# Optimization experiments

Hardware: AMD Instinct MI355X
Metric: run time of the kernel (lower is better)

The kernel has to match this reference:

```python
import jax, jax.numpy as jnp
import numpy as np

EPS = 1e-5

def layer_norm(x, g, b):
    mu = jnp.mean(x, axis=-1, keepdims=True)
    var = jnp.mean(jnp.square(x - mu), axis=-1, keepdims=True)
    return (x - mu) * jax.lax.rsqrt(var + EPS) * g + b

def setup_inputs() -> dict:
    key = jax.random.key(0)
    ks = jax.random.split(key, 8)
    B, N, C, H = 1, 384, 128, 128
    s = 0.02
    return {
        "pair": jax.random.normal(ks[0], (B, N, N, C), dtype=jnp.float32),
        "ln_l_g": jnp.ones((C,), jnp.float32), "ln_l_b": jnp.zeros((C,), jnp.float32),
        "ln_r_g": jnp.ones((C,), jnp.float32), "ln_r_b": jnp.zeros((C,), jnp.float32),
        "Wl": jax.random.normal(ks[1], (C, H), jnp.float32) * s, "bl": jnp.zeros((H,), jnp.float32),
        "Wr": jax.random.normal(ks[2], (C, H), jnp.float32) * s, "br": jnp.zeros((H,), jnp.float32),
        "Wg": jax.random.normal(ks[3], (C, H), jnp.float32) * s, "bg": jnp.zeros((H,), jnp.float32),
        "Wo": jax.random.normal(ks[4], (H, C), jnp.float32) * s, "bo": jnp.zeros((C,), jnp.float32),
        "n_g": jnp.ones((C,), jnp.float32), "n_b": jnp.zeros((C,), jnp.float32),
    }

def reference(pair, ln_l_g, ln_l_b, ln_r_g, ln_r_b, Wl, bl, Wr, br, Wg, bg, Wo, bo, n_g, n_b):
    # pair: [B, N, N, C]
    left = layer_norm(pair, ln_l_g, ln_l_b) @ Wl + bl      # [B,N,N,H]
    right = layer_norm(pair, ln_r_g, ln_r_b) @ Wr + br     # [B,N,N,H]
    gate = jax.nn.sigmoid(pair @ Wg + bg)                  # [B,N,N,H]
    # triangle multiplicative update: per-channel N x N matmul over k
    out = jnp.einsum('bikh,bkjh->bijh', left, right)
    out = out * gate
    out = out @ Wo + bo                                    # [B,N,N,C]
    return layer_norm(out + pair, n_g, n_b)
```

## Files before the change

kernel.cpp:

```cpp
#include <hip/hip_runtime.h>
#include <hip/hip_bf16.h>

#define N_ 384
#define C_ 128
#define M_ (N_*N_)

typedef __attribute__((ext_vector_type(8))) short bf16x8_t;
typedef __attribute__((ext_vector_type(4))) float f32x4_t;
typedef unsigned int u32;
typedef unsigned short u16;
typedef unsigned long long u64;

__device__ __forceinline__ u16 f2bf(float f) {
  u32 u = __builtin_bit_cast(u32, f);
  u32 r = (u + 0x7FFFu + ((u >> 16) & 1u)) >> 16;
  return (u16)r;
}
__device__ __forceinline__ float bf2f(u16 h) {
  u32 u = ((u32)h) << 16;
  return __builtin_bit_cast(float, u);
}

__global__ __launch_bounds__(256) void k_prep1(const float* __restrict__ lg, const float* __restrict__ rg,
    const float* __restrict__ Wl, const float* __restrict__ Wr, const float* __restrict__ Wg,
    const float* __restrict__ Wo, u16* __restrict__ wcat, u16* __restrict__ wot) {
  int idx = blockIdx.x*256 + threadIdx.x;
  if (idx < 49152) {
    int n = idx >> 7, k = idx & 127;
    float v;
    if (n < 128)      v = lg[k] * Wl[k*128 + n];
    else if (n < 256) v = rg[k] * Wr[k*128 + (n-128)];
    else              v = Wg[k*128 + (n-256)];
    wcat[idx] = f2bf(v);
  } else {
    int i2 = idx - 49152;
    int c = i2 >> 7, h = i2 & 127;
    wot[i2] = f2bf(Wo[h*128 + c]);
  }
}

__global__ __launch_bounds__(512) void k_prep2(const float* __restrict__ lb, const float* __restrict__ rb,
    const float* __restrict__ Wl, const float* __restrict__ Wr, const float* __restrict__ Wg,
    const float* __restrict__ bl, const float* __restrict__ br, const float* __restrict__ bg,
    float* __restrict__ bcat, float* __restrict__ sg) {
  int t = threadIdx.x;
  if (blockIdx.x == 0) {
    if (t < 384) {
      float s = 0.f;
      if (t < 128)      { for (int k=0;k<128;k++) s += lb[k]*Wl[k*128+t];       s += bl[t];     }
      else if (t < 256) { int h=t-128; for (int k=0;k<128;k++) s += rb[k]*Wr[k*128+h]; s += br[h]; }
      else              { s = bg[t-256]; }
      bcat[t] = s;
    }
  } else {
    if (t < 128) {
      float s = 0.f;
      for (int k=0;k<128;k++) s += Wg[k*128+t];
      sg[t] = s;
    }
  }
}

#define LDK 136
#define LDA 72
#define LDW 72

__global__ __launch_bounds__(512) void k_projln(const float* __restrict__ pair,
    const u16* __restrict__ wcat, const float* __restrict__ bcat, const float* __restrict__ sg,
    u16* __restrict__ left_t, u16* __restrict__ right_t, u16* __restrict__ gate_t) {
  __shared__ u16 At[128*LDK];
  __shared__ float mu_s[128];
  __shared__ float irs_s[128];
  int bx = blockIdx.x;
  int r0 = bx * 128;
  int t = threadIdx.x, w = t>>6, lane = t&63;
  int q = lane>>4, nl = lane&15;

  {
    int rr = t >> 2, quarter = t & 3;
    const float4* gp = (const float4*)(pair + (size_t)(r0+rr)*128 + quarter*32);
    float4 v[8];
    #pragma unroll
    for (int i=0;i<8;i++) v[i] = gp[i];
    float s=0.f, qq=0.f;
    #pragma unroll
    for (int i=0;i<8;i++) {
      s  += v[i].x + v[i].y + v[i].z + v[i].w;
      qq += v[i].x*v[i].x + v[i].y*v[i].y + v[i].z*v[i].z + v[i].w*v[i].w;
    }
    s  += __shfl_xor(s, 1, 64);
    s  += __shfl_xor(s, 2, 64);
    qq += __shfl_xor(qq, 1, 64);
    qq += __shfl_xor(qq, 2, 64);
    float mu = s * (1.f/128.f);
    float var = qq*(1.f/128.f) - mu*mu;
    float rstd = rsqrtf(var + 1e-5f);
    if (quarter == 0) { mu_s[rr] = mu; irs_s[rr] = 1.0f/rstd; }
    u32* lp = (u32*)(At + rr*LDK + quarter*32);
    #pragma unroll
    for (int i=0;i<4;i++) {
      u32 p0 = (u32)f2bf((v[2*i].x-mu)*rstd)   | ((u32)f2bf((v[2*i].y-mu)*rstd)<<16);
      u32 p1 = (u32)f2bf((v[2*i].z-mu)*rstd)   | ((u32)f2bf((v[2*i].w-mu)*rstd)<<16);
      u32 p2 = (u32)f2bf((v[2*i+1].x-mu)*rstd) | ((u32)f2bf((v[2*i+1].y-mu)*rstd)<<16);
      u32 p3 = (u32)f2bf((v[2*i+1].z-mu)*rstd) | ((u32)f2bf((v[2*i+1].w-mu)*rstd)<<16);
      ((uint4*)lp)[i] = make_uint4(p0,p1,p2,p3);
    }
  }
  __syncthreads();

  #pragma unroll 1
  for (int nb = 0; nb < 3; ++nb) {
    const u16* bbase = wcat + (size_t)(nb*128)*128;
    f32x4_t acc[8] = {};
    #pragma unroll
    for (int ks=0; ks<4; ks++) {
      int kel = ks*32 + q*8;
      bf16x8_t b = *(const bf16x8_t*)(bbase + (size_t)(w*16 + nl)*128 + kel);
      #pragma unroll
      for (int tm=0;tm<8;tm++) {
        bf16x8_t a = *(const bf16x8_t*)(At + (tm*16+nl)*LDK + kel);
        acc[tm] = __builtin_amdgcn_mfma_f32_16x16x32_bf16(a, b, acc[tm], 0,0,0);
      }
    }
    u16* dst = (nb==0) ? left_t : (nb==1) ? right_t : gate_t;
    int n = w*16 + nl;
    float bias = bcat[nb*128 + n];
    u16* rowp = dst + (size_t)n*M_ + r0;
    if (nb == 2) {
      float sgn = sg[n];
      #pragma unroll
      for (int tm=0;tm<8;tm++) {
        f32x4_t mu4 = *(const f32x4_t*)(mu_s  + tm*16 + q*4);
        f32x4_t ir4 = *(const f32x4_t*)(irs_s + tm*16 + q*4);
        float v0 = acc[tm][0]*ir4[0] + mu4[0]*sgn + bias;
        float v1 = acc[tm][1]*ir4[1] + mu4[1]*sgn + bias;
        float v2 = acc[tm][2]*ir4[2] + mu4[2]*sgn + bias;
        float v3 = acc[tm][3]*ir4[3] + mu4[3]*sgn + bias;
        v0 = 1.0f/(1.0f+__expf(-v0));
        v1 = 1.0f/(1.0f+__expf(-v1));
        v2 = 1.0f/(1.0f+__expf(-v2));
        v3 = 1.0f/(1.0f+__expf(-v3));
        u32 pk0 = (u32)f2bf(v0) | ((u32)f2bf(v1)<<16);
        u32 pk1 = (u32)f2bf(v2) | ((u32)f2bf(v3)<<16);
        *(u64*)(rowp + tm*16 + q*4) = (u64)pk0 | ((u64)pk1<<32);
      }
    } else {
      #pragma unroll
      for (int tm=0;tm<8;tm++) {
        u32 pk0 = (u32)f2bf(acc[tm][0]+bias) | ((u32)f2bf(acc[tm][1]+bias)<<16);
        u32 pk1 = (u32)f2bf(acc[tm][2]+bias) | ((u32)f2bf(acc[tm][3]+bias)<<16);
        *(u64*)(rowp + tm*16 + q*4) = (u64)pk0 | ((u64)pk1<<32);
      }
    }
  }
}

__global__ __launch_bounds__(256) void k_einsum(const u16* __restrict__ left_t, const u16* __restrict__ right_t,
    const u16* __restrict__ gate_t, u16* __restrict__ og_t) {
  __shared__ u16 smem[2*128*LDA];
  u16* At = smem; u16* Bt = smem + 128*LDA;
  int bx = blockIdx.x;
  int wk = (bx & 7) * 144 + (bx >> 3);
  int h = wk / 9; int rem = wk % 9;
  int i0 = (rem/3)*128, j0 = (rem%3)*128;
  const u16* Ag = left_t + (size_t)h*M_;
  const u16* Bg = right_t + (size_t)h*M_;
  int t = threadIdx.x, w = t>>6, lane = t&63;
  int q = lane>>4, nl = lane&15;
  f32x4_t acc[4][4] = {};
  int m0 = (w&1)*64, n0 = (w>>1)*64;
  for (int kb = 0; kb < N_; kb += 64) {
    {
      int rr = t>>1, half = t&1;
      const u16* gp = Ag + (size_t)(i0+rr)*N_ + kb + half*32;
      u16* lp = At + rr*LDA + half*32;
      #pragma unroll
      for (int i=0;i<4;i++) ((uint4*)lp)[i] = ((const uint4*)gp)[i];
    }
    {
      int kk2 = t>>3;
      int seg = t&7;
      const u16* g0 = Bg + (size_t)(kb + 2*kk2)*N_ + j0 + seg*16;
      const u16* g1 = g0 + N_;
      uint4 r0a = ((const uint4*)g0)[0], r0b = ((const uint4*)g0)[1];
      uint4 r1a = ((const uint4*)g1)[0], r1b = ((const uint4*)g1)[1];
      u32 w0[8] = {r0a.x,r0a.y,r0a.z,r0a.w,r0b.x,r0b.y,r0b.z,r0b.w};
      u32 w1[8] = {r1a.x,r1a.y,r1a.z,r1a.w,r1b.x,r1b.y,r1b.z,r1b.w};
      u32 sw = (u32)seg << 4;
      char* bbytes = (char*)Bt;
      #pragma unroll
      for (int e=0;e<8;e++) {
        u32 lo = w0[e], hi = w1[e];
        u32 evenw = (lo & 0xffffu) | (hi << 16);
        u32 oddw  = (lo >> 16)     | (hi & 0xffff0000u);
        int je = seg*16 + 2*e;
        u32 byteE = ((u32)(je*LDA + 2*kk2) * 2u) ^ sw;
        u32 byteO = ((u32)((je+1)*LDA + 2*kk2) * 2u) ^ sw;
        *(u32*)(bbytes + byteE) = evenw;
        *(u32*)(bbytes + byteO) = oddw;
      }
    }
    __syncthreads();
    for (int ks=0; ks<2; ks++) {
      int kel = ks*32 + q*8;
      bf16x8_t a[4], b[4];
      #pragma unroll
      for (int tm=0;tm<4;tm++) a[tm] = *(const bf16x8_t*)(At + (m0+tm*16+nl)*LDA + kel);
      #pragma unroll
      for (int tn=0;tn<4;tn++) {
        u32 swr = (u32)(((n0>>4) + tn) & 7) << 4;
        b[tn] = *(const bf16x8_t*)((const char*)Bt + ((u32)(((n0+tn*16+nl)*LDA + kel)*2) ^ swr));
      }
      #pragma unroll
      for (int tm=0;tm<4;tm++)
        #pragma unroll
        for (int tn=0;tn<4;tn++)
          acc[tm][tn] = __builtin_amdgcn_mfma_f32_16x16x32_bf16(a[tm], b[tn], acc[tm][tn], 0,0,0);
    }
    __syncthreads();
  }
#define LDT 136
  u16* Ot = smem;
  #pragma unroll
  for (int tm=0;tm<4;tm++)
    #pragma unroll
    for (int tn=0;tn<4;tn++)
      #pragma unroll
      for (int p=0;p<4;p++) {
        int m = m0 + tm*16 + q*4 + p;
        int n = n0 + tn*16 + nl;
        Ot[m*LDT + n] = f2bf(acc[tm][tn][p]);
      }
  __syncthreads();
  {
    int m = t>>1, half = t&1;
    size_t rbase = (size_t)h*M_ + (size_t)(i0+m)*N_ + j0 + half*64;
    const uint4* gg = (const uint4*)(gate_t + rbase);
    const uint4* lo = (const uint4*)(Ot + m*LDT + half*64);
    uint4* od = (uint4*)(og_t + rbase);
    #pragma unroll
    for (int i=0;i<8;i++) {
      uint4 gv = gg[i]; uint4 ov = lo[i];
      u32 ga[4] = {gv.x,gv.y,gv.z,gv.w};
      u32 oa[4] = {ov.x,ov.y,ov.z,ov.w};
      u32 ra[4];
      #pragma unroll
      for (int e=0;e<4;e++) {
        float g0 = bf2f((u16)(ga[e]&0xffffu)), g1 = bf2f((u16)(ga[e]>>16));
        float o0 = bf2f((u16)(oa[e]&0xffffu)), o1 = bf2f((u16)(oa[e]>>16));
        ra[e] = (u32)f2bf(o0*g0) | ((u32)f2bf(o1*g1)<<16);
      }
      od[i] = make_uint4(ra[0],ra[1],ra[2],ra[3]);
    }
  }
}

__global__ __launch_bounds__(256) void k_final(const u16* __restrict__ og_t, const u16* __restrict__ wot,
    const float* __restrict__ pair, const float* __restrict__ bo,
    const float* __restrict__ ng, const float* __restrict__ nb_,
    float* __restrict__ out) {
  __shared__ u16 smem[2*128*LDW];
  u16* At = smem; u16* Wt = smem + 128*LDW;
  int bx = blockIdx.x;
  int r0 = bx * 128;
  int t = threadIdx.x, w = t>>6, lane = t&63;
  int q = lane>>4, nl = lane&15;
  f32x4_t acc[2][8] = {};
  for (int c0 = 0; c0 < 128; c0 += 64) {
    {
      int hh = t>>2, seg = t&3;
      const u16* gp = og_t + (size_t)(c0+hh)*M_ + r0 + seg*32;
      uint4 bb[4];
      #pragma unroll
      for (int i=0;i<4;i++) bb[i] = ((const uint4*)gp)[i];
      #pragma unroll
      for (int i=0;i<4;i++) {
        int rb = seg*32 + i*8;
        u32 x0=bb[i].x, x1=bb[i].y, x2=bb[i].z, x3=bb[i].w;
        At[(rb+0)*LDW+hh] = (u16)(x0&0xffffu); At[(rb+1)*LDW+hh] = (u16)(x0>>16);
        At[(rb+2)*LDW+hh] = (u16)(x1&0xffffu); At[(rb+3)*LDW+hh] = (u16)(x1>>16);
        At[(rb+4)*LDW+hh] = (u16)(x2&0xffffu); At[(rb+5)*LDW+hh] = (u16)(x2>>16);
        At[(rb+6)*LDW+hh] = (u16)(x3&0xffffu); At[(rb+7)*LDW+hh] = (u16)(x3>>16);
      }
    }
    {
      int c = t>>1, half = t&1;
      const u16* gp = wot + (size_t)c*128 + c0 + half*32;
      u16* lp = Wt + c*LDW + half*32;
      #pragma unroll
      for (int i=0;i<4;i++) ((uint4*)lp)[i] = ((const uint4*)gp)[i];
    }
    __syncthreads();
    int mbase = w*32;
    for (int ks=0; ks<2; ks++) {
      int kel = ks*32 + q*8;
      bf16x8_t a[2], b[8];
      #pragma unroll
      for (int tm=0;tm<2;tm++) a[tm] = *(const bf16x8_t*)(At + (mbase+tm*16+nl)*LDW + kel);
      #pragma unroll
      for (int tn=0;tn<8;tn++) b[tn] = *(const bf16x8_t*)(Wt + (tn*16+nl)*LDW + kel);
      #pragma unroll
      for (int tm=0;tm<2;tm++)
        #pragma unroll
        for (int tn=0;tn<8;tn++)
          acc[tm][tn] = __builtin_amdgcn_mfma_f32_16x16x32_bf16(a[tm], b[tn], acc[tm][tn], 0,0,0);
    }
    __syncthreads();
  }
  float rsum[2][4], rsq[2][4];
  for (int tm=0;tm<2;tm++) for (int p=0;p<4;p++) { rsum[tm][p]=0.f; rsq[tm][p]=0.f; }
  #pragma unroll
  for (int tm=0;tm<2;tm++)
    #pragma unroll
    for (int tn=0;tn<8;tn++) {
      int n = tn*16 + nl;
      float bb = bo[n];
      #pragma unroll
      for (int p=0;p<4;p++) {
        int m = w*32 + tm*16 + q*4 + p;
        float v = acc[tm][tn][p] + bb + pair[(size_t)(r0+m)*128 + n];
        acc[tm][tn][p] = v;
        rsum[tm][p] += v;
        rsq[tm][p]  += v*v;
      }
    }
  for (int msk=1; msk<16; msk<<=1) {
    #pragma unroll
    for (int tm=0;tm<2;tm++)
      #pragma unroll
      for (int p=0;p<4;p++) {
        rsum[tm][p] += __shfl_xor(rsum[tm][p], msk, 64);
        rsq[tm][p]  += __shfl_xor(rsq[tm][p],  msk, 64);
      }
  }
  #pragma unroll
  for (int tm=0;tm<2;tm++)
    #pragma unroll
    for (int p=0;p<4;p++) {
      float mu = rsum[tm][p] * (1.f/128.f);
      float var = rsq[tm][p]*(1.f/128.f) - mu*mu;
      rsum[tm][p] = mu;
      rsq[tm][p] = rsqrtf(var + 1e-5f);
    }
  #pragma unroll
  for (int tm=0;tm<2;tm++)
    #pragma unroll
    for (int tn=0;tn<8;tn++) {
      int n = tn*16 + nl;
      float g = ng[n], b2 = nb_[n];
      #pragma unroll
      for (int p=0;p<4;p++) {
        int m = w*32 + tm*16 + q*4 + p;
        out[(size_t)(r0+m)*128 + n] = (acc[tm][tn][p] - rsum[tm][p]) * rsq[tm][p] * g + b2;
      }
    }
}

extern "C" void kernel_launch(void* const* d_in, const int* in_sizes, int n_in,
                              void* d_out, int out_size, void* d_ws, size_t ws_size,
                              hipStream_t stream) {
  (void)in_sizes; (void)n_in; (void)out_size; (void)ws_size;
  const float* pair   = (const float*)d_in[0];
  const float* ln_l_g = (const float*)d_in[1];
  const float* ln_l_b = (const float*)d_in[2];
  const float* ln_r_g = (const float*)d_in[3];
  const float* ln_r_b = (const float*)d_in[4];
  const float* Wl = (const float*)d_in[5];
  const float* bl = (const float*)d_in[6];
  const float* Wr = (const float*)d_in[7];
  const float* br = (const float*)d_in[8];
  const float* Wg = (const float*)d_in[9];
  const float* bg = (const float*)d_in[10];
  const float* Wo = (const float*)d_in[11];
  const float* bo = (const float*)d_in[12];
  const float* n_g = (const float*)d_in[13];
  const float* n_b = (const float*)d_in[14];

  char* ws = (char*)d_ws;
  const size_t SZ = (size_t)M_*128*sizeof(u16);
  u16*  og_t    = (u16*)(ws);
  u16*  gate_t  = (u16*)(ws + SZ);
  u16*  wcat    = (u16*)(ws + 2*SZ);
  float* bcat   = (float*)(ws + 2*SZ + 98304);
  float* sgp    = (float*)(ws + 2*SZ + 98304 + 1536);
  u16*  wot     = (u16*)(ws + 2*SZ + 98304 + 1536 + 512);

  u16* left_t   = (u16*)d_out;
  u16* right_t  = (u16*)d_out + (size_t)M_*128;

  k_prep1<<<256, 256, 0, stream>>>(ln_l_g, ln_r_g, Wl, Wr, Wg, Wo, wcat, wot);
  k_prep2<<<2, 512, 0, stream>>>(ln_l_b, ln_r_b, Wl, Wr, Wg, bl, br, bg, bcat, sgp);
  k_projln<<<1152, 512, 0, stream>>>(pair, wcat, bcat, sgp, left_t, right_t, gate_t);
  k_einsum<<<1152, 256, 0, stream>>>(left_t, right_t, gate_t, og_t);
  k_final<<<1152, 256, 0, stream>>>(og_t, wot, pair, bo, n_g, n_b, (float*)d_out);
}
```

Measured before the change: 279.4 us.

## Double threads per block in einsum and final kernels, merge prep kernels

The einsum and final GEMM kernels now run 512 threads (8 waves) per block instead of 256. Each wave owns a smaller output tile, so accumulators and register pressure shrink. Global-to-LDS loads and the epilogue are redistributed across the extra threads. The two weight-prep kernels are also merged into one launch to save launch overhead. In exchange, each wave reuses fragments less (smaller tiles per wave) and block-wide barriers cover more waves.

```diff
diff --git a/kernel.cpp b/kernel.cpp
--- a/kernel.cpp
+++ b/kernel.cpp
@@ -21,49 +21,42 @@
   return __builtin_bit_cast(float, u);
 }
 
-__global__ __launch_bounds__(256) void k_prep1(const float* __restrict__ lg, const float* __restrict__ rg,
+__global__ __launch_bounds__(256) void k_prep(const float* __restrict__ lg, const float* __restrict__ rg,
     const float* __restrict__ Wl, const float* __restrict__ Wr, const float* __restrict__ Wg,
-    const float* __restrict__ Wo, u16* __restrict__ wcat, u16* __restrict__ wot) {
-  int idx = blockIdx.x*256 + threadIdx.x;
-  if (idx < 49152) {
-    int n = idx >> 7, k = idx & 127;
-    float v;
-    if (n < 128)      v = lg[k] * Wl[k*128 + n];
-    else if (n < 256) v = rg[k] * Wr[k*128 + (n-128)];
-    else              v = Wg[k*128 + (n-256)];
-    wcat[idx] = f2bf(v);
+    const float* __restrict__ Wo,
+    const float* __restrict__ lb, const float* __restrict__ rb,
+    const float* __restrict__ bl, const float* __restrict__ br, const float* __restrict__ bg,
+    u16* __restrict__ wcat, u16* __restrict__ wot,
+    float* __restrict__ bcat, float* __restrict__ sg) {
+  int bx = blockIdx.x, t = threadIdx.x;
+  if (bx < 256) {
+    int idx = bx*256 + t;
+    if (idx < 49152) {
+      int n = idx >> 7, k = idx & 127;
+      float v;
+      if (n < 128)      v = lg[k] * Wl[k*128 + n];
+      else if (n < 256) v = rg[k] * Wr[k*128 + (n-128)];
+      else              v = Wg[k*128 + (n-256)];
+      wcat[idx] = f2bf(v);
+    } else {
+      int i2 = idx - 49152;
+      int c = i2 >> 7, h = i2 & 127;
+      wot[i2] = f2bf(Wo[h*128 + c]);
+    }
+  } else if (bx == 256) {
+    float s = 0.f;
+    if (t < 128)      { for (int k=0;k<128;k++) s += lb[k]*Wl[k*128+t];       s += bl[t];     bcat[t] = s; }
+    else              { int hh=t-128; for (int k=0;k<128;k++) s += rb[k]*Wr[k*128+hh]; s += br[hh]; bcat[t] = s; }
   } else {
-    int i2 = idx - 49152;
-    int c = i2 >> 7, h = i2 & 127;
-    wot[i2] = f2bf(Wo[h*128 + c]);
-  }
-}
-
-__global__ __launch_bounds__(512) void k_prep2(const float* __restrict__ lb, const float* __restrict__ rb,
-    const float* __restrict__ Wl, const float* __restrict__ Wr, const float* __restrict__ Wg,
-    const float* __restrict__ bl, const float* __restrict__ br, const float* __restrict__ bg,
-    float* __restrict__ bcat, float* __restrict__ sg) {
-  int t = threadIdx.x;
-  if (blockIdx.x == 0) {
-    if (t < 384) {
-      float s = 0.f;
-      if (t < 128)      { for (int k=0;k<128;k++) s += lb[k]*Wl[k*128+t];       s += bl[t];     }
-      else if (t < 256) { int h=t-128; for (int k=0;k<128;k++) s += rb[k]*Wr[k*128+h]; s += br[h]; }
-      else              { s = bg[t-256]; }
-      bcat[t] = s;
-    }
-  } else {
-    if (t < 128) {
-      float s = 0.f;
-      for (int k=0;k<128;k++) s += Wg[k*128+t];
-      sg[t] = s;
-    }
+    if (t < 128)      { bcat[256+t] = bg[t]; }
+    else              { int hh = t-128; float s=0.f; for (int k=0;k<128;k++) s += Wg[k*128+hh]; sg[hh] = s; }
   }
 }
 
 #define LDK 136
 #define LDA 72
 #define LDW 72
+#define LDT 136
 
 __global__ __launch_bounds__(512) void k_projln(const float* __restrict__ pair,
     const u16* __restrict__ wcat, const float* __restrict__ bcat, const float* __restrict__ sg,
@@ -155,7 +148,7 @@
   }
 }
 
-__global__ __launch_bounds__(256) void k_einsum(const u16* __restrict__ left_t, const u16* __restrict__ right_t,
+__global__ __launch_bounds__(512) void k_einsum(const u16* __restrict__ left_t, const u16* __restrict__ right_t,
     const u16* __restrict__ gate_t, u16* __restrict__ og_t) {
   __shared__ u16 smem[2*128*LDA];
   u16* At = smem; u16* Bt = smem + 128*LDA;
@@ -167,33 +160,33 @@
   const u16* Bg = right_t + (size_t)h*M_;
   int t = threadIdx.x, w = t>>6, lane = t&63;
   int q = lane>>4, nl = lane&15;
-  f32x4_t acc[4][4] = {};
-  int m0 = (w&1)*64, n0 = (w>>1)*64;
+  f32x4_t acc[4][2] = {};
+  int m0 = (w&1)*64, nb0 = (w>>1)*32;
   for (int kb = 0; kb < N_; kb += 64) {
     {
-      int rr = t>>1, half = t&1;
-      const u16* gp = Ag + (size_t)(i0+rr)*N_ + kb + half*32;
-      u16* lp = At + rr*LDA + half*32;
-      #pragma unroll
-      for (int i=0;i<4;i++) ((uint4*)lp)[i] = ((const uint4*)gp)[i];
+      int rr = t>>2, quarter = t&3;
+      const u16* gp = Ag + (size_t)(i0+rr)*N_ + kb + quarter*16;
+      u16* lp = At + rr*LDA + quarter*16;
+      ((uint4*)lp)[0] = ((const uint4*)gp)[0];
+      ((uint4*)lp)[1] = ((const uint4*)gp)[1];
     }
     {
-      int kk2 = t>>3;
-      int seg = t&7;
-      const u16* g0 = Bg + (size_t)(kb + 2*kk2)*N_ + j0 + seg*16;
+      int kk2 = t>>4;
+      int seg = t&15;
+      const u16* g0 = Bg + (size_t)(kb + 2*kk2)*N_ + j0 + seg*8;
       const u16* g1 = g0 + N_;
-      uint4 r0a = ((const uint4*)g0)[0], r0b = ((const uint4*)g0)[1];
-      uint4 r1a = ((const uint4*)g1)[0], r1b = ((const uint4*)g1)[1];
-      u32 w0[8] = {r0a.x,r0a.y,r0a.z,r0a.w,r0b.x,r0b.y,r0b.z,r0b.w};
-      u32 w1[8] = {r1a.x,r1a.y,r1a.z,r1a.w,r1b.x,r1b.y,r1b.z,r1b.w};
-      u32 sw = (u32)seg << 4;
+      uint4 ra = ((const uint4*)g0)[0];
+      uint4 rbv = ((const uint4*)g1)[0];
+      u32 w0[4] = {ra.x,ra.y,ra.z,ra.w};
+      u32 w1[4] = {rbv.x,rbv.y,rbv.z,rbv.w};
+      u32 sw = (u32)(seg>>1) << 4;
       char* bbytes = (char*)Bt;
       #pragma unroll
-      for (int e=0;e<8;e++) {
+      for (int e=0;e<4;e++) {
         u32 lo = w0[e], hi = w1[e];
         u32 evenw = (lo & 0xffffu) | (hi << 16);
         u32 oddw  = (lo >> 16)     | (hi & 0xffff0000u);
-        int je = seg*16 + 2*e;
+        int je = seg*8 + 2*e;
         u32 byteE = ((u32)(je*LDA + 2*kk2) * 2u) ^ sw;
         u32 byteO = ((u32)((je+1)*LDA + 2*kk2) * 2u) ^ sw;
         *(u32*)(bbytes + byteE) = evenw;
@@ -201,61 +194,61 @@
       }
     }
     __syncthreads();
+    #pragma unroll
     for (int ks=0; ks<2; ks++) {
       int kel = ks*32 + q*8;
-      bf16x8_t a[4], b[4];
+      bf16x8_t a[4], b[2];
       #pragma unroll
       for (int tm=0;tm<4;tm++) a[tm] = *(const bf16x8_t*)(At + (m0+tm*16+nl)*LDA + kel);
       #pragma unroll
-      for (int tn=0;tn<4;tn++) {
-        u32 swr = (u32)(((n0>>4) + tn) & 7) << 4;
-        b[tn] = *(const bf16x8_t*)((const char*)Bt + ((u32)(((n0+tn*16+nl)*LDA + kel)*2) ^ swr));
+      for (int tn=0;tn<2;tn++) {
+        u32 swr = (u32)(((nb0>>4) + tn) & 7) << 4;
+        b[tn] = *(const bf16x8_t*)((const char*)Bt + ((u32)(((nb0+tn*16+nl)*LDA + kel)*2) ^ swr));
       }
       #pragma unroll
       for (int tm=0;tm<4;tm++)
         #pragma unroll
-        for (int tn=0;tn<4;tn++)
+        for (int tn=0;tn<2;tn++)
           acc[tm][tn] = __builtin_amdgcn_mfma_f32_16x16x32_bf16(a[tm], b[tn], acc[tm][tn], 0,0,0);
     }
     __syncthreads();
   }
-#define LDT 136
   u16* Ot = smem;
   #pragma unroll
   for (int tm=0;tm<4;tm++)
     #pragma unroll
-    for (int tn=0;tn<4;tn++)
+    for (int tn=0;tn<2;tn++)
       #pragma unroll
       for (int p=0;p<4;p++) {
         int m = m0 + tm*16 + q*4 + p;
-        int n = n0 + tn*16 + nl;
+        int n = nb0 + tn*16 + nl;
         Ot[m*LDT + n] = f2bf(acc[tm][tn][p]);
       }
   __syncthreads();
   {
-    int m = t>>1, half = t&1;
-    size_t rbase = (size_t)h*M_ + (size_t)(i0+m)*N_ + j0 + half*64;
+    int m = t>>2, hq = t&3;
+    size_t rbase = (size_t)h*M_ + (size_t)(i0+m)*N_ + j0 + hq*32;
     const uint4* gg = (const uint4*)(gate_t + rbase);
-    const uint4* lo = (const uint4*)(Ot + m*LDT + half*64);
+    const uint4* lo = (const uint4*)(Ot + m*LDT + hq*32);
     uint4* od = (uint4*)(og_t + rbase);
     #pragma unroll
-    for (int i=0;i<8;i++) {
+    for (int i=0;i<4;i++) {
       uint4 gv = gg[i]; uint4 ov = lo[i];
       u32 ga[4] = {gv.x,gv.y,gv.z,gv.w};
       u32 oa[4] = {ov.x,ov.y,ov.z,ov.w};
-      u32 ra[4];
+      u32 ra2[4];
       #pragma unroll
       for (int e=0;e<4;e++) {
         float g0 = bf2f((u16)(ga[e]&0xffffu)), g1 = bf2f((u16)(ga[e]>>16));
         float o0 = bf2f((u16)(oa[e]&0xffffu)), o1 = bf2f((u16)(oa[e]>>16));
-        ra[e] = (u32)f2bf(o0*g0) | ((u32)f2bf(o1*g1)<<16);
-      }
-      od[i] = make_uint4(ra[0],ra[1],ra[2],ra[3]);
-    }
-  }
-}
-
-__global__ __launch_bounds__(256) void k_final(const u16* __restrict__ og_t, const u16* __restrict__ wot,
+        ra2[e] = (u32)f2bf(o0*g0) | ((u32)f2bf(o1*g1)<<16);
+      }
+      od[i] = make_uint4(ra2[0],ra2[1],ra2[2],ra2[3]);
+    }
+  }
+}
+
+__global__ __launch_bounds__(512) void k_final(const u16* __restrict__ og_t, const u16* __restrict__ wot,
     const float* __restrict__ pair, const float* __restrict__ bo,
     const float* __restrict__ ng, const float* __restrict__ nb_,
     float* __restrict__ out) {
@@ -265,95 +258,84 @@
   int r0 = bx * 128;
   int t = threadIdx.x, w = t>>6, lane = t&63;
   int q = lane>>4, nl = lane&15;
-  f32x4_t acc[2][8] = {};
+  f32x4_t acc[8] = {};
+  int m0 = w*16;
   for (int c0 = 0; c0 < 128; c0 += 64) {
     {
-      int hh = t>>2, seg = t&3;
-      const u16* gp = og_t + (size_t)(c0+hh)*M_ + r0 + seg*32;
-      uint4 bb[4];
-      #pragma unroll
-      for (int i=0;i<4;i++) bb[i] = ((const uint4*)gp)[i];
-      #pragma unroll
-      for (int i=0;i<4;i++) {
-        int rb = seg*32 + i*8;
-        u32 x0=bb[i].x, x1=bb[i].y, x2=bb[i].z, x3=bb[i].w;
-        At[(rb+0)*LDW+hh] = (u16)(x0&0xffffu); At[(rb+1)*LDW+hh] = (u16)(x0>>16);
-        At[(rb+2)*LDW+hh] = (u16)(x1&0xffffu); At[(rb+3)*LDW+hh] = (u16)(x1>>16);
-        At[(rb+4)*LDW+hh] = (u16)(x2&0xffffu); At[(rb+5)*LDW+hh] = (u16)(x2>>16);
-        At[(rb+6)*LDW+hh] = (u16)(x3&0xffffu); At[(rb+7)*LDW+hh] = (u16)(x3>>16);
+      int hh = t>>3, seg = t&7;
+      const u16* gp = og_t + (size_t)(c0+hh)*M_ + r0 + seg*16;
+      uint4 b0 = ((const uint4*)gp)[0];
+      uint4 b1 = ((const uint4*)gp)[1];
+      u32 xs[8] = {b0.x,b0.y,b0.z,b0.w,b1.x,b1.y,b1.z,b1.w};
+      #pragma unroll
+      for (int e=0;e<8;e++) {
+        int rb = seg*16 + 2*e;
+        At[(rb+0)*LDW+hh] = (u16)(xs[e]&0xffffu);
+        At[(rb+1)*LDW+hh] = (u16)(xs[e]>>16);
       }
     }
     {
-      int c = t>>1, half = t&1;
-      const u16* gp = wot + (size_t)c*128 + c0 + half*32;
-      u16* lp = Wt + c*LDW + half*32;
-      #pragma unroll
-      for (int i=0;i<4;i++) ((uint4*)lp)[i] = ((const uint4*)gp)[i];
+      int c = t>>2, q4 = t&3;
+      const u16* gp = wot + (size_t)c*128 + c0 + q4*16;
+      u16* lp = Wt + c*LDW + q4*16;
+      ((uint4*)lp)[0] = ((const uint4*)gp)[0];
+      ((uint4*)lp)[1] = ((const uint4*)gp)[1];
     }
     __syncthreads();
-    int mbase = w*32;
+    #pragma unroll
     for (int ks=0; ks<2; ks++) {
       int kel = ks*32 + q*8;
-      bf16x8_t a[2], b[8];
-      #pragma unroll
-      for (int tm=0;tm<2;tm++) a[tm] = *(const bf16x8_t*)(At + (mbase+tm*16+nl)*LDW + kel);
+      bf16x8_t a = *(const bf16x8_t*)(At + (m0+nl)*LDW + kel);
+      bf16x8_t b[8];
       #pragma unroll
       for (int tn=0;tn<8;tn++) b[tn] = *(const bf16x8_t*)(Wt + (tn*16+nl)*LDW + kel);
       #pragma unroll
-      for (int tm=0;tm<2;tm++)
-        #pragma unroll
-        for (int tn=0;tn<8;tn++)
-          acc[tm][tn] = __builtin_amdgcn_mfma_f32_16x16x32_bf16(a[tm], b[tn], acc[tm][tn], 0,0,0);
+      for (int tn=0;tn<8;tn++)
+        acc[tn] = __builtin_amdgcn_mfma_f32_16x16x32_bf16(a, b[tn], acc[tn], 0,0,0);
     }
     __syncthreads();
   }
-  float rsum[2][4], rsq[2][4];
-  for (int tm=0;tm<2;tm++) for (int p=0;p<4;p++) { rsum[tm][p]=0.f; rsq[tm][p]=0.f; }
-  #pragma unroll
-  for (int tm=0;tm<2;tm++)
-    #pragma unroll
-    for (int tn=0;tn<8;tn++) {
-      int n = tn*16 + nl;
-      float bb = bo[n];
-      #pragma unroll
-      for (int p=0;p<4;p++) {
-        int m = w*32 + tm*16 + q*4 + p;
-        float v = acc[tm][tn][p] + bb + pair[(size_t)(r0+m)*128 + n];
-        acc[tm][tn][p] = v;
-        rsum[tm][p] += v;
-        rsq[tm][p]  += v*v;
-      }
-    }
+  float rsum[4], rsq[4];
+  #pragma unroll
+  for (int p=0;p<4;p++) { rsum[p]=0.f; rsq[p]=0.f; }
+  #pragma unroll
+  for (int tn=0;tn<8;tn++) {
+    int n = tn*16 + nl;
+    float bb = bo[n];
+    #pragma unroll
+    for (int p=0;p<4;p++) {
+      int m = m0 + q*4 + p;
+      float v = acc[tn][p] + bb + pair[(size_t)(r0+m)*128 + n];
+      acc[tn][p] = v;
+      rsum[p] += v;
+      rsq[p]  += v*v;
+    }
+  }
+  #pragma unroll
   for (int msk=1; msk<16; msk<<=1) {
     #pragma unroll
-    for (int tm=0;tm<2;tm++)
-      #pragma unroll
-      for (int p=0;p<4;p++) {
-        rsum[tm][p] += __shfl_xor(rsum[tm][p], msk, 64);
-        rsq[tm][p]  += __shfl_xor(rsq[tm][p],  msk, 64);
-      }
-  }
-  #pragma unroll
-  for (int tm=0;tm<2;tm++)
-    #pragma unroll
     for (int p=0;p<4;p++) {
-      float mu = rsum[tm][p] * (1.f/128.f);
-      float var = rsq[tm][p]*(1.f/128.f) - mu*mu;
-      rsum[tm][p] = mu;
-      rsq[tm][p] = rsqrtf(var + 1e-5f);
-    }
-  #pragma unroll
-  for (int tm=0;tm<2;tm++)
-    #pragma unroll
-    for (int tn=0;tn<8;tn++) {
-      int n = tn*16 + nl;
-      float g = ng[n], b2 = nb_[n];
-      #pragma unroll
-      for (int p=0;p<4;p++) {
-        int m = w*32 + tm*16 + q*4 + p;
-        out[(size_t)(r0+m)*128 + n] = (acc[tm][tn][p] - rsum[tm][p]) * rsq[tm][p] * g + b2;
-      }
-    }
+      rsum[p] += __shfl_xor(rsum[p], msk, 64);
+      rsq[p]  += __shfl_xor(rsq[p],  msk, 64);
+    }
+  }
+  #pragma unroll
+  for (int p=0;p<4;p++) {
+    float mu = rsum[p] * (1.f/128.f);
+    float var = rsq[p]*(1.f/128.f) - mu*mu;
+    rsum[p] = mu;
+    rsq[p] = rsqrtf(var + 1e-5f);
+  }
+  #pragma unroll
+  for (int tn=0;tn<8;tn++) {
+    int n = tn*16 + nl;
+    float g = ng[n], b2 = nb_[n];
+    #pragma unroll
+    for (int p=0;p<4;p++) {
+      int m = m0 + q*4 + p;
+      out[(size_t)(r0+m)*128 + n] = (acc[tn][p] - rsum[p]) * rsq[p] * g + b2;
+    }
+  }
 }
 
 extern "C" void kernel_launch(void* const* d_in, const int* in_sizes, int n_in,
@@ -388,9 +370,9 @@
   u16* left_t   = (u16*)d_out;
   u16* right_t  = (u16*)d_out + (size_t)M_*128;
 
-  k_prep1<<<256, 256, 0, stream>>>(ln_l_g, ln_r_g, Wl, Wr, Wg, Wo, wcat, wot);
-  k_prep2<<<2, 512, 0, stream>>>(ln_l_b, ln_r_b, Wl, Wr, Wg, bl, br, bg, bcat, sgp);
+  k_prep<<<258, 256, 0, stream>>>(ln_l_g, ln_r_g, Wl, Wr, Wg, Wo,
+                                  ln_l_b, ln_r_b, bl, br, bg, wcat, wot, bcat, sgp);
   k_projln<<<1152, 512, 0, stream>>>(pair, wcat, bcat, sgp, left_t, right_t, gate_t);
-  k_einsum<<<1152, 256, 0, stream>>>(left_t, right_t, gate_t, og_t);
-  k_final<<<1152, 256, 0, stream>>>(og_t, wot, pair, bo, n_g, n_b, (float*)d_out);
-}
+  k_einsum<<<1152, 512, 0, stream>>>(left_t, right_t, gate_t, og_t);
+  k_final<<<1152, 512, 0, stream>>>(og_t, wot, pair, bo, n_g, n_b, (float*)d_out);
+}
```

Measured after the change: 271.4 us. 2.9% less time.
